# Optimization experiments

Measured on AMD Instinct MI355X. Metric: run time of the kernel, lower is better.

The kernel has to match this reference:

```python
import jax, jax.numpy as jnp
import numpy as np

N_HEAD = 12
SCALING = 0.17677669529663687  # 1/sqrt(head_dim=32)


def setup_inputs() -> dict:
    key = jax.random.key(0)
    ks = jax.random.split(key, 6)
    B, R, C, E = 1, 256, 384, 384
    s = 1.0 / np.sqrt(E)
    return {
        "x": jax.random.normal(ks[0], (B, R, C, E), dtype=jnp.float32),
        "Wq": (jax.random.normal(ks[1], (E, E), dtype=jnp.float32) * s),
        "Wk": (jax.random.normal(ks[2], (E, E), dtype=jnp.float32) * s),
        "Wv": (jax.random.normal(ks[3], (E, E), dtype=jnp.float32) * s),
        "Wq_s": (jax.random.normal(ks[4], (E, E), dtype=jnp.float32) * s),
        "Wk_s": (jax.random.normal(ks[5], (E, E), dtype=jnp.float32) * s),
        "res_mask": jnp.ones((B, C), dtype=jnp.int32),
        "seq_mask": jnp.ones((B, R), dtype=jnp.int32),
    }


def reference(x, Wq, Wk, Wv, Wq_s, Wk_s, res_mask, seq_mask):
    B, R, C, E = x.shape
    H = N_HEAD
    D = E // H
    NEG = jnp.finfo(x.dtype).min

    # ---- SeqWeightAttention: per-column attention over rows, query = row 0 ----
    scale_s = 1.0 / np.sqrt(D)
    msa = jnp.transpose(x, (0, 2, 1, 3))                 # [B,C,R,E]
    q0 = msa[:, :, 0]                                    # [B,C,E]
    Qs = (q0 @ Wq_s).reshape(B, C, 1, H, D)
    Qs = jnp.transpose(Qs, (0, 1, 3, 2, 4)) * scale_s    # [B,C,H,1,D]
    Ks = (msa @ Wk_s).reshape(B, C, R, H, D)
    Ks = jnp.transpose(Ks, (0, 1, 3, 4, 2))              # [B,C,H,D,R]
    QKs = Qs @ Ks                                        # [B,C,H,1,R]
    QKs = jnp.where(seq_mask[:, None, None, None, :] == 0, NEG, QKs)
    sw = jax.nn.softmax(QKs, axis=-1)
    sw = jnp.transpose(sw, (0, 4, 1, 2, 3))              # [B,R,C,H,1]

    # ---- main attention, row-contracted (attn_seq_weight path) ----
    scaling = SCALING / np.sqrt(C)                        # seqlen_scaling=True
    Q = (x @ Wq).reshape(B, R, C, H, D) * scaling * sw    # Q modulated by seq weights
    K = (x @ Wk).reshape(B, R, C, H, D)
    V = (x @ Wv).reshape(B, R, C, H, D)

    QK = jnp.einsum('brihd,brjhd->bhij', Q, K)            # contract rows + head_dim
    rm = res_mask[:, :, None] * res_mask[:, None, :]      # [B,C,C]
    QK = jnp.where(rm[:, None, :, :] == 0, NEG, QK)
    attn = jax.nn.softmax(QK, axis=-1)                    # [B,H,C,C]

    out = jnp.einsum('bhij,brjhd->brihd', attn, V)
    return out.reshape(B, R, C, E)
```

## Files before the change

### kernel.cpp

```cpp
#include <hip/hip_runtime.h>
#include <math.h>
#include <stdint.h>

#define DEV_INLINE __device__ __forceinline__

constexpr int R_ = 256, C_ = 384, E_ = 384, H_ = 12, D_ = 32;
constexpr float NEGF = -3.402823466e38f;

typedef __attribute__((ext_vector_type(4))) float f32x4;
typedef __attribute__((ext_vector_type(8))) short short8;
typedef __attribute__((ext_vector_type(4))) unsigned short u16x4;

constexpr size_t o_qs     = 0;
constexpr size_t o_p      = o_qs + (size_t)C_ * E_;
constexpr size_t o_logits = o_p + (size_t)C_ * H_ * E_;
constexpr size_t o_sw     = o_logits + (size_t)C_ * H_ * R_;
constexpr size_t o_attn   = o_sw + (size_t)C_ * H_ * R_;
constexpr size_t o_q3     = o_attn + (size_t)H_ * C_ * C_;
constexpr size_t SZBIG  = 75497472;
constexpr size_t ob_q3b = o_q3 * 4;
constexpr size_t ob_k3b = ob_q3b + SZBIG;
constexpr size_t ob_v3b = ob_k3b + SZBIG;
constexpr size_t ob_xb  = ob_v3b + SZBIG;

DEV_INLINE unsigned short bf16h(float x) {
  unsigned int u = __builtin_bit_cast(unsigned int, x);
  unsigned int r = (u + 0x7FFFu + ((u >> 16) & 1u)) >> 16;
  return (unsigned short)r;
}
DEV_INLINE float waveRedMax(float v) {
#pragma unroll
  for (int o = 32; o > 0; o >>= 1) v = fmaxf(v, __shfl_down(v, o));
  return v;
}
DEV_INLINE float waveRedSum(float v) {
#pragma unroll
  for (int o = 32; o > 0; o >>= 1) v += __shfl_down(v, o);
  return v;
}

DEV_INLINE void gll16(const void* g, void* l) {
  __builtin_amdgcn_global_load_lds(
      reinterpret_cast<__attribute__((address_space(1))) void*>(
          reinterpret_cast<uintptr_t>(g)),
      reinterpret_cast<__attribute__((address_space(3))) void*>(
          reinterpret_cast<uintptr_t>(l)),
      16, 0, 0);
}

template <int ROWS, int UPR, int MASK>
DEV_INLINE void stageT(const unsigned short* __restrict__ g, int lda,
                       unsigned short* l) {
  int t = threadIdx.x, w = t >> 6, lane = t & 63;
  constexpr int NI = (ROWS * UPR) / 64;
  constexpr int PW = NI / 4;
#pragma unroll
  for (int j = 0; j < PW; ++j) {
    int u0 = (w * PW + j) * 64;
    int u = u0 + lane;
    int row = u / UPR, qp = u % UPR;
    int q = qp ^ (row & MASK);
    gll16(g + (size_t)row * lda + q * 8, l + (size_t)u0 * 8);
  }
}

template <int MASK>
DEV_INLINE short8 fragLd(const unsigned short* base, int row, int q, int rowShorts) {
  int qp = q ^ (row & MASK);
  return *(const short8*)(base + row * rowShorts + qp * 8);
}

__global__ void k_qs(const float* __restrict__ x, const float* __restrict__ Wq_s,
                     float* __restrict__ ws) {
  int c = blockIdx.x, t = threadIdx.x;
  __shared__ float xl[E_];
  xl[t] = x[(size_t)c * E_ + t];
  __syncthreads();
  float s = 0.f;
#pragma unroll 8
  for (int k = 0; k < E_; ++k) s += xl[k] * Wq_s[(size_t)k * E_ + t];
  ws[o_qs + (size_t)c * E_ + t] = s * 0.17677669529663687f;
}

__global__ void k_p(const float* __restrict__ Wk_s, const float* __restrict__ ws,
                    unsigned short* __restrict__ Pb) {
  int h = blockIdx.x, c = blockIdx.y, t = threadIdx.x;
  __shared__ float q[D_];
  float s = 0.f;
  if (h < 12) {
    if (t < D_) q[t] = ws[o_qs + (size_t)c * E_ + h * D_ + t];
    __syncthreads();
    const float* wrow = &Wk_s[(size_t)t * E_ + h * D_];
#pragma unroll
    for (int d = 0; d < D_; d += 4) {
      float4 w = *(const float4*)&wrow[d];
      s += w.x * q[d] + w.y * q[d + 1] + w.z * q[d + 2] + w.w * q[d + 3];
    }
  }
  Pb[((size_t)c * 16 + h) * 384 + t] = bf16h(s);
}

__global__ __launch_bounds__(256) void k_logits_sm(
    const unsigned short* __restrict__ xb, const unsigned short* __restrict__ Pb,
    const int* __restrict__ seq_mask, float* __restrict__ swT) {
  int c = blockIdx.x, t = threadIdx.x;
  __shared__ unsigned short sA[256 * 32];
  __shared__ unsigned short sB[16 * 32];
  __shared__ float lg[12 * 256];
  __shared__ float red[4];
  int w = t >> 6, lane = t & 63, id16 = lane & 15, g = lane >> 4;
  f32x4 acc[4];
#pragma unroll
  for (int mi = 0; mi < 4; ++mi) acc[mi] = (f32x4){0.f, 0.f, 0.f, 0.f};

  for (int k0 = 0; k0 < 384; k0 += 32) {
    stageT<256, 4, 3>(xb + (size_t)c * 384 + k0, 384 * 384, sA);
    if (w == 0) {
      int row = lane >> 2, qp = lane & 3, q = qp ^ (row & 3);
      gll16(Pb + ((size_t)c * 16 + row) * 384 + k0 + q * 8, sB);
    }
    __syncthreads();
    short8 Bf = fragLd<3>(sB, id16, g, 32);
#pragma unroll
    for (int mi = 0; mi < 4; ++mi) {
      short8 Af = fragLd<3>(sA, w * 64 + mi * 16 + id16, g, 32);
      acc[mi] = __builtin_amdgcn_mfma_f32_16x16x32_bf16(Af, Bf, acc[mi], 0, 0, 0);
    }
    __syncthreads();
  }
  int l4 = (lane >> 4) * 4;
#pragma unroll
  for (int mi = 0; mi < 4; ++mi) {
    if (id16 < 12) {
      f32x4 a = acc[mi];
#pragma unroll
      for (int reg = 0; reg < 4; ++reg)
        lg[id16 * 256 + w * 64 + mi * 16 + l4 + reg] = a[reg];
    }
  }
  __syncthreads();
  int wid = t >> 6;
  const float scal = 0.17677669529663687f / sqrtf((float)C_);
  bool masked = (seq_mask[t] == 0);
  for (int h = 0; h < 12; ++h) {
    float v = masked ? NEGF : lg[h * 256 + t];
    float m = waveRedMax(v);
    if ((t & 63) == 0) red[wid] = m;
    __syncthreads();
    float mx = fmaxf(fmaxf(red[0], red[1]), fmaxf(red[2], red[3]));
    __syncthreads();
    float e = expf(v - mx);
    float s = waveRedSum(e);
    if ((t & 63) == 0) red[wid] = s;
    __syncthreads();
    float sum = red[0] + red[1] + red[2] + red[3];
    swT[((size_t)h * 256 + t) * 384 + c] = e / sum * scal;
    __syncthreads();
  }
}

__global__ void k_cvt_x(const float* __restrict__ x, unsigned short* __restrict__ xb) {
  size_t i = ((size_t)blockIdx.x * 256 + threadIdx.x) * 16;
  unsigned short h[16];
#pragma unroll
  for (int j = 0; j < 4; ++j) {
    float4 f = *(const float4*)&x[i + j * 4];
    h[j * 4 + 0] = bf16h(f.x);
    h[j * 4 + 1] = bf16h(f.y);
    h[j * 4 + 2] = bf16h(f.z);
    h[j * 4 + 3] = bf16h(f.w);
  }
  *(short8*)&xb[i] = *(const short8*)&h[0];
  *(short8*)&xb[i + 8] = *(const short8*)&h[8];
}

__global__ void k_cvt_w(const float* __restrict__ Wq, const float* __restrict__ Wk,
                        const float* __restrict__ Wv, unsigned short* __restrict__ Wtb) {
  int n = blockIdx.x, k = threadIdx.x;
  const float* W;
  int col;
  if (n < 384)      { W = Wq; col = n; }
  else if (n < 768) { W = Wk; col = n - 384; }
  else              { W = Wv; col = n - 768; }
  Wtb[(size_t)n * 384 + k] = bf16h(W[(size_t)k * 384 + col]);
}

__global__ __launch_bounds__(256, 4) void k_proj_all(
    const unsigned short* __restrict__ xb, const unsigned short* __restrict__ Wtb,
    const float* __restrict__ swT, unsigned short* __restrict__ Q3b,
    unsigned short* __restrict__ K3b, unsigned short* __restrict__ V3b) {
  __shared__ unsigned short sA[128 * 64], sB[128 * 64];
  int Dd = blockIdx.x;
  int L = (Dd & 7) * 864 + (Dd >> 3);
  int bm = L / 9, bn = L - bm * 9;
  int n0 = bn * 128, m0 = bm * 128;
  int wave = threadIdx.x >> 6, wr = wave >> 1, wc = wave & 1;
  int lane = threadIdx.x & 63, id16 = lane & 15, g = lane >> 4;
  f32x4 acc[4][4];
#pragma unroll
  for (int mi = 0; mi < 4; ++mi)
#pragma unroll
    for (int ni = 0; ni < 4; ++ni) acc[mi][ni] = (f32x4){0.f, 0.f, 0.f, 0.f};

  for (int it = 0; it < 6; ++it) {
    stageT<128, 8, 7>(xb + (size_t)m0 * 384 + it * 64, 384, sA);
    stageT<128, 8, 7>(Wtb + (size_t)n0 * 384 + it * 64, 384, sB);
    __syncthreads();
    short8 Af[4][2], Bf[4][2];
#pragma unroll
    for (int mi = 0; mi < 4; ++mi) {
      int row = wr * 64 + mi * 16 + id16;
#pragma unroll
      for (int kk = 0; kk < 2; ++kk) Af[mi][kk] = fragLd<7>(sA, row, kk * 4 + g, 64);
    }
#pragma unroll
    for (int ni = 0; ni < 4; ++ni) {
      int col = wc * 64 + ni * 16 + id16;
#pragma unroll
      for (int kk = 0; kk < 2; ++kk) Bf[ni][kk] = fragLd<7>(sB, col, kk * 4 + g, 64);
    }
#pragma unroll
    for (int kk = 0; kk < 2; ++kk)
#pragma unroll
      for (int mi = 0; mi < 4; ++mi)
#pragma unroll
        for (int ni = 0; ni < 4; ++ni)
          acc[mi][ni] = __builtin_amdgcn_mfma_f32_16x16x32_bf16(Af[mi][kk], Bf[ni][kk],
                                                                acc[mi][ni], 0, 0, 0);
    __syncthreads();
  }

  int l4 = (lane >> 4) * 4;
  int r = bm / 3, cb = (bm % 3) * 128;
  if (bn < 6) {
#pragma unroll
    for (int mi = 0; mi < 4; ++mi) {
      int cbase = cb + wr * 64 + mi * 16 + l4;
#pragma unroll
      for (int ni = 0; ni < 4; ++ni) {
        int n = n0 + wc * 64 + ni * 16 + id16;
        bool isQ = n < 384;
        int nn = isQ ? n : n - 384;
        int hh = nn >> 5, dd = nn & 31;
        f32x4 a = acc[mi][ni];
        if (isQ) {
          float4 sv = *(const float4*)&swT[((size_t)hh * 256 + r) * 384 + cbase];
          a[0] *= sv.x; a[1] *= sv.y; a[2] *= sv.z; a[3] *= sv.w;
        }
        unsigned short* dst = isQ ? Q3b : K3b;
#pragma unroll
        for (int reg = 0; reg < 4; ++reg)
          dst[((size_t)(hh * 384 + cbase + reg)) * 8192 + r * 32 + dd] = bf16h(a[reg]);
      }
    }
  } else {
#pragma unroll
    for (int mi = 0; mi < 4; ++mi) {
      int c0 = cb + wr * 64 + mi * 16 + l4;
#pragma unroll
      for (int ni = 0; ni < 4; ++ni) {
        int nv = n0 + wc * 64 + ni * 16 + id16 - 768;
        int hh = nv >> 5, dd = nv & 31;
        f32x4 a = acc[mi][ni];
        u16x4 hv;
#pragma unroll
        for (int reg = 0; reg < 4; ++reg) hv[reg] = bf16h(a[reg]);
        *(u16x4*)(V3b + ((size_t)hh * 8192 + r * 32 + dd) * 384 + c0) = hv;
      }
    }
  }
}

__global__ __launch_bounds__(256, 4) void k_qk_mma(
    const unsigned short* __restrict__ Q3b, const unsigned short* __restrict__ K3b,
    float* __restrict__ QKf0, float* __restrict__ QKf1) {
  __shared__ unsigned short sA[64 * 128], sB[64 * 128];
  int Dd = blockIdx.x;
  int L = (Dd & 7) * 108 + (Dd >> 3);
  int kh = L / 432, rem = L - kh * 432;
  int h = rem / 36, r2 = rem - h * 36, bi = r2 / 6, bj = r2 - bi * 6;
  int wave = threadIdx.x >> 6, wr = wave >> 1, wc = wave & 1;
  int lane = threadIdx.x & 63, id16 = lane & 15, g = lane >> 4;
  f32x4 acc[2][2];
#pragma unroll
  for (int mi = 0; mi < 2; ++mi)
#pragma unroll
    for (int ni = 0; ni < 2; ++ni) acc[mi][ni] = (f32x4){0.f, 0.f, 0.f, 0.f};
  const unsigned short* Ab =
      Q3b + (size_t)h * 384 * 8192 + (size_t)(bi * 64) * 8192 + kh * 4096;
  const unsigned short* Bb =
      K3b + (size_t)h * 384 * 8192 + (size_t)(bj * 64) * 8192 + kh * 4096;

  for (int it = 0; it < 32; ++it) {
    stageT<64, 16, 7>(Ab + it * 128, 8192, sA);
    stageT<64, 16, 7>(Bb + it * 128, 8192, sB);
    __syncthreads();
    short8 Af[2][4], Bf[2][4];
#pragma unroll
    for (int mi = 0; mi < 2; ++mi) {
      int row = wr * 32 + mi * 16 + id16;
#pragma unroll
      for (int kk = 0; kk < 4; ++kk) Af[mi][kk] = fragLd<7>(sA, row, kk * 4 + g, 128);
    }
#pragma unroll
    for (int ni = 0; ni < 2; ++ni) {
      int col = wc * 32 + ni * 16 + id16;
#pragma unroll
      for (int kk = 0; kk < 4; ++kk) Bf[ni][kk] = fragLd<7>(sB, col, kk * 4 + g, 128);
    }
#pragma unroll
    for (int kk = 0; kk < 4; ++kk)
#pragma unroll
      for (int mi = 0; mi < 2; ++mi)
#pragma unroll
        for (int ni = 0; ni < 2; ++ni)
          acc[mi][ni] = __builtin_amdgcn_mfma_f32_16x16x32_bf16(Af[mi][kk], Bf[ni][kk],
                                                                acc[mi][ni], 0, 0, 0);
    __syncthreads();
  }
  int l4 = (lane >> 4) * 4;
  float* dst = kh ? QKf1 : QKf0;
#pragma unroll
  for (int mi = 0; mi < 2; ++mi)
#pragma unroll
    for (int ni = 0; ni < 2; ++ni) {
      int i0 = bi * 64 + wr * 32 + mi * 16 + l4;
      int j = bj * 64 + wc * 32 + ni * 16 + id16;
      f32x4 a = acc[mi][ni];
#pragma unroll
      for (int reg = 0; reg < 4; ++reg)
        dst[((size_t)h * 384 + i0 + reg) * 384 + j] = a[reg];
    }
}

__global__ void k_softmax_j(const int* __restrict__ res_mask, const float* __restrict__ QKf0,
                            const float* __restrict__ QKf1,
                            unsigned short* __restrict__ attnb) {
  int i = blockIdx.x, h = blockIdx.y, t = threadIdx.x;
  int lane = t & 63, wid = t >> 6;
  size_t base = ((size_t)h * C_ + i) * C_;
  float v = QKf0[base + t] + QKf1[base + t];
  if ((res_mask[i] * res_mask[t]) == 0) v = NEGF;
  __shared__ float red[6];
  float m = waveRedMax(v);
  if (lane == 0) red[wid] = m;
  __syncthreads();
  float mx = red[0];
#pragma unroll
  for (int w = 1; w < 6; ++w) mx = fmaxf(mx, red[w]);
  __syncthreads();
  float e = expf(v - mx);
  float s = waveRedSum(e);
  if (lane == 0) red[wid] = s;
  __syncthreads();
  float sum = 0.f;
#pragma unroll
  for (int w = 0; w < 6; ++w) sum += red[w];
  attnb[base + t] = bf16h(e / sum);
}

__global__ __launch_bounds__(256, 4) void k_out_mma(
    const unsigned short* __restrict__ attnb, const unsigned short* __restrict__ V3b,
    float* __restrict__ out) {
  __shared__ unsigned short sA[128 * 64], sB[128 * 64];
  int Dd = blockIdx.x;
  int L = (Dd & 7) * 288 + (Dd >> 3);
  int bn = L % 64, bm = (L / 64) % 3, h = L / 192;
  int n0 = bn * 128, m0 = bm * 128;
  int wave = threadIdx.x >> 6, wr = wave >> 1, wc = wave & 1;
  int lane = threadIdx.x & 63, id16 = lane & 15, g = lane >> 4;
  f32x4 acc[4][4];
#pragma unroll
  for (int mi = 0; mi < 4; ++mi)
#pragma unroll
    for (int ni = 0; ni < 4; ++ni) acc[mi][ni] = (f32x4){0.f, 0.f, 0.f, 0.f};
  const unsigned short* Ab = attnb + (size_t)h * 384 * 384 + (size_t)m0 * 384;
  const unsigned short* Bb = V3b + (size_t)h * 8192 * 384 + (size_t)n0 * 384;

  for (int it = 0; it < 6; ++it) {
    stageT<128, 8, 7>(Ab + it * 64, 384, sA);
    stageT<128, 8, 7>(Bb + it * 64, 384, sB);
    __syncthreads();
    short8 Af[4][2], Bf[4][2];
#pragma unroll
    for (int mi = 0; mi < 4; ++mi) {
      int row = wr * 64 + mi * 16 + id16;
#pragma unroll
      for (int kk = 0; kk < 2; ++kk) Af[mi][kk] = fragLd<7>(sA, row, kk * 4 + g, 64);
    }
#pragma unroll
    for (int ni = 0; ni < 4; ++ni) {
      int col = wc * 64 + ni * 16 + id16;
#pragma unroll
      for (int kk = 0; kk < 2; ++kk) Bf[ni][kk] = fragLd<7>(sB, col, kk * 4 + g, 64);
    }
#pragma unroll
    for (int kk = 0; kk < 2; ++kk)
#pragma unroll
      for (int mi = 0; mi < 4; ++mi)
#pragma unroll
        for (int ni = 0; ni < 4; ++ni)
          acc[mi][ni] = __builtin_amdgcn_mfma_f32_16x16x32_bf16(Af[mi][kk], Bf[ni][kk],
                                                                acc[mi][ni], 0, 0, 0);
    __syncthreads();
  }
  int l4 = (lane >> 4) * 4;
#pragma unroll
  for (int mi = 0; mi < 4; ++mi)
#pragma unroll
    for (int ni = 0; ni < 4; ++ni) {
      int i0 = m0 + wr * 64 + mi * 16 + l4;
      int n = n0 + wc * 64 + ni * 16 + id16;
      int r = n >> 5, d = n & 31;
      f32x4 a = acc[mi][ni];
#pragma unroll
      for (int reg = 0; reg < 4; ++reg)
        out[(((size_t)r * 384 + i0 + reg) * 12 + h) * 32 + d] = a[reg];
    }
}

extern "C" void kernel_launch(void* const* d_in, const int* in_sizes, int n_in,
                              void* d_out, int out_size, void* d_ws, size_t ws_size,
                              hipStream_t stream) {
  const float* x = (const float*)d_in[0];
  const float* Wq = (const float*)d_in[1];
  const float* Wk = (const float*)d_in[2];
  const float* Wv = (const float*)d_in[3];
  const float* Wq_s = (const float*)d_in[4];
  const float* Wk_s = (const float*)d_in[5];
  const int* res_mask = (const int*)d_in[6];
  const int* seq_mask = (const int*)d_in[7];
  float* ws = (float*)d_ws;
  char* wsb = (char*)d_ws;
  float* out = (float*)d_out;

  unsigned short* Pb  = (unsigned short*)(wsb + o_p * 4);
  float* swT          = ws + o_logits;
  unsigned short* Wtb = (unsigned short*)(wsb + o_attn * 4);
  float* QKf0         = ws + o_attn;
  unsigned short* Q3b = (unsigned short*)(wsb + ob_q3b);
  unsigned short* K3b = (unsigned short*)(wsb + ob_k3b);
  unsigned short* V3b = (unsigned short*)(wsb + ob_v3b);
  unsigned short* xb  = (unsigned short*)(wsb + ob_xb);
  unsigned short* attnb = Q3b;
  float* QKf1 = (float*)(wsb + ob_xb);

  hipLaunchKernelGGL(k_cvt_x, dim3(9216), dim3(256), 0, stream, x, xb);
  hipLaunchKernelGGL(k_qs, dim3(C_), dim3(E_), 0, stream, x, Wq_s, ws);
  hipLaunchKernelGGL(k_p, dim3(16, C_), dim3(E_), 0, stream, Wk_s, ws, Pb);
  hipLaunchKernelGGL(k_logits_sm, dim3(C_), dim3(256), 0, stream, xb, Pb, seq_mask, swT);
  hipLaunchKernelGGL(k_cvt_w, dim3(1152), dim3(384), 0, stream, Wq, Wk, Wv, Wtb);
  hipLaunchKernelGGL(k_proj_all, dim3(6912), dim3(256), 0, stream, xb, Wtb, swT,
                     Q3b, K3b, V3b);
  hipLaunchKernelGGL(k_qk_mma, dim3(864), dim3(256), 0, stream, Q3b, K3b, QKf0, QKf1);
  hipLaunchKernelGGL(k_softmax_j, dim3(C_, H_), dim3(C_), 0, stream, res_mask,
                     QKf0, QKf1, attnb);
  hipLaunchKernelGGL(k_out_mma, dim3(2304), dim3(256), 0, stream, attnb, V3b, out);
}
```

Baseline: 411.8 us.

## Change Q/K layout to head-row-column-dim and retile QK GEMM to 128x128

The projection epilogue now stages Q and K tiles in shared memory and writes them as contiguous 16-byte chunks in an [h][r][c][d] layout instead of scattered 2-byte stores with an 8192 stride. The QK kernel is rewritten to consume that layout, using 128x128 output tiles and staging two rows of 32 head-dim values per iteration, with a shifted swizzle to suit 64-byte rows. This cuts the grid from 864 to 216 blocks, which lowers occupancy on a chip with many CUs, in exchange for more data reuse per block and coalesced projection stores.

```diff
diff --git a/kernel.cpp b/kernel.cpp
--- a/kernel.cpp
+++ b/kernel.cpp
@@ -48,7 +48,7 @@
       16, 0, 0);
 }
 
-template <int ROWS, int UPR, int MASK>
+template <int ROWS, int UPR, int MASK, int SHIFT>
 DEV_INLINE void stageT(const unsigned short* __restrict__ g, int lda,
                        unsigned short* l) {
   int t = threadIdx.x, w = t >> 6, lane = t & 63;
@@ -59,14 +59,14 @@
     int u0 = (w * PW + j) * 64;
     int u = u0 + lane;
     int row = u / UPR, qp = u % UPR;
-    int q = qp ^ (row & MASK);
+    int q = qp ^ ((row >> SHIFT) & MASK);
     gll16(g + (size_t)row * lda + q * 8, l + (size_t)u0 * 8);
   }
 }
 
-template <int MASK>
+template <int MASK, int SHIFT>
 DEV_INLINE short8 fragLd(const unsigned short* base, int row, int q, int rowShorts) {
-  int qp = q ^ (row & MASK);
+  int qp = q ^ ((row >> SHIFT) & MASK);
   return *(const short8*)(base + row * rowShorts + qp * 8);
 }
 
@@ -114,16 +114,16 @@
   for (int mi = 0; mi < 4; ++mi) acc[mi] = (f32x4){0.f, 0.f, 0.f, 0.f};
 
   for (int k0 = 0; k0 < 384; k0 += 32) {
-    stageT<256, 4, 3>(xb + (size_t)c * 384 + k0, 384 * 384, sA);
+    stageT<256, 4, 3, 0>(xb + (size_t)c * 384 + k0, 384 * 384, sA);
     if (w == 0) {
       int row = lane >> 2, qp = lane & 3, q = qp ^ (row & 3);
       gll16(Pb + ((size_t)c * 16 + row) * 384 + k0 + q * 8, sB);
     }
     __syncthreads();
-    short8 Bf = fragLd<3>(sB, id16, g, 32);
+    short8 Bf = fragLd<3, 0>(sB, id16, g, 32);
 #pragma unroll
     for (int mi = 0; mi < 4; ++mi) {
-      short8 Af = fragLd<3>(sA, w * 64 + mi * 16 + id16, g, 32);
+      short8 Af = fragLd<3, 0>(sA, w * 64 + mi * 16 + id16, g, 32);
       acc[mi] = __builtin_amdgcn_mfma_f32_16x16x32_bf16(Af, Bf, acc[mi], 0, 0, 0);
     }
     __syncthreads();
@@ -189,7 +189,9 @@
     const unsigned short* __restrict__ xb, const unsigned short* __restrict__ Wtb,
     const float* __restrict__ swT, unsigned short* __restrict__ Q3b,
     unsigned short* __restrict__ K3b, unsigned short* __restrict__ V3b) {
-  __shared__ unsigned short sA[128 * 64], sB[128 * 64];
+  __shared__ unsigned short smem[2 * 128 * 64];
+  unsigned short* sA = smem;
+  unsigned short* sB = smem + 128 * 64;
   int Dd = blockIdx.x;
   int L = (Dd & 7) * 864 + (Dd >> 3);
   int bm = L / 9, bn = L - bm * 9;
@@ -203,21 +205,21 @@
     for (int ni = 0; ni < 4; ++ni) acc[mi][ni] = (f32x4){0.f, 0.f, 0.f, 0.f};
 
   for (int it = 0; it < 6; ++it) {
-    stageT<128, 8, 7>(xb + (size_t)m0 * 384 + it * 64, 384, sA);
-    stageT<128, 8, 7>(Wtb + (size_t)n0 * 384 + it * 64, 384, sB);
+    stageT<128, 8, 7, 0>(xb + (size_t)m0 * 384 + it * 64, 384, sA);
+    stageT<128, 8, 7, 0>(Wtb + (size_t)n0 * 384 + it * 64, 384, sB);
     __syncthreads();
     short8 Af[4][2], Bf[4][2];
 #pragma unroll
     for (int mi = 0; mi < 4; ++mi) {
       int row = wr * 64 + mi * 16 + id16;
 #pragma unroll
-      for (int kk = 0; kk < 2; ++kk) Af[mi][kk] = fragLd<7>(sA, row, kk * 4 + g, 64);
+      for (int kk = 0; kk < 2; ++kk) Af[mi][kk] = fragLd<7, 0>(sA, row, kk * 4 + g, 64);
     }
 #pragma unroll
     for (int ni = 0; ni < 4; ++ni) {
       int col = wc * 64 + ni * 16 + id16;
 #pragma unroll
-      for (int kk = 0; kk < 2; ++kk) Bf[ni][kk] = fragLd<7>(sB, col, kk * 4 + g, 64);
+      for (int kk = 0; kk < 2; ++kk) Bf[ni][kk] = fragLd<7, 0>(sB, col, kk * 4 + g, 64);
     }
 #pragma unroll
     for (int kk = 0; kk < 2; ++kk)
@@ -233,30 +235,41 @@
   int l4 = (lane >> 4) * 4;
   int r = bm / 3, cb = (bm % 3) * 128;
   if (bn < 6) {
+    bool isQ = bn < 3;
+    int hbase = isQ ? bn * 4 : (bn - 3) * 4;
 #pragma unroll
     for (int mi = 0; mi < 4; ++mi) {
-      int cbase = cb + wr * 64 + mi * 16 + l4;
+      int clBase = wr * 64 + mi * 16 + l4;
 #pragma unroll
       for (int ni = 0; ni < 4; ++ni) {
-        int n = n0 + wc * 64 + ni * 16 + id16;
-        bool isQ = n < 384;
-        int nn = isQ ? n : n - 384;
-        int hh = nn >> 5, dd = nn & 31;
+        int nl = wc * 64 + ni * 16 + id16;
+        int hhl = nl >> 5, d = nl & 31;
         f32x4 a = acc[mi][ni];
         if (isQ) {
-          float4 sv = *(const float4*)&swT[((size_t)hh * 256 + r) * 384 + cbase];
+          float4 sv =
+              *(const float4*)&swT[((size_t)(hbase + hhl) * 256 + r) * 384 + cb + clBase];
           a[0] *= sv.x; a[1] *= sv.y; a[2] *= sv.z; a[3] *= sv.w;
         }
-        unsigned short* dst = isQ ? Q3b : K3b;
 #pragma unroll
         for (int reg = 0; reg < 4; ++reg)
-          dst[((size_t)(hh * 384 + cbase + reg)) * 8192 + r * 32 + dd] = bf16h(a[reg]);
+          smem[hhl * 4096 + (clBase + reg) * 32 + d] = bf16h(a[reg]);
       }
     }
+    __syncthreads();
+    unsigned short* dst = isQ ? Q3b : K3b;
+#pragma unroll
+    for (int seg = 0; seg < 8; ++seg) {
+      int off = seg * 2048 + threadIdx.x * 8;
+      int hhl = off >> 12, inner = off & 4095;
+      int hg = hbase + hhl;
+      *(short8*)(dst + (((size_t)hg * 256 + r) * 384 + cb) * 32 + inner) =
+          *(const short8*)(smem + off);
+    }
   } else {
+    int r2 = r, cb2 = cb;
 #pragma unroll
     for (int mi = 0; mi < 4; ++mi) {
-      int c0 = cb + wr * 64 + mi * 16 + l4;
+      int c0 = cb2 + wr * 64 + mi * 16 + l4;
 #pragma unroll
       for (int ni = 0; ni < 4; ++ni) {
         int nv = n0 + wc * 64 + ni * 16 + id16 - 768;
@@ -265,7 +278,7 @@
         u16x4 hv;
 #pragma unroll
         for (int reg = 0; reg < 4; ++reg) hv[reg] = bf16h(a[reg]);
-        *(u16x4*)(V3b + ((size_t)hh * 8192 + r * 32 + dd) * 384 + c0) = hv;
+        *(u16x4*)(V3b + ((size_t)hh * 8192 + r2 * 32 + dd) * 384 + c0) = hv;
       }
     }
   }
@@ -274,62 +287,60 @@
 __global__ __launch_bounds__(256, 4) void k_qk_mma(
     const unsigned short* __restrict__ Q3b, const unsigned short* __restrict__ K3b,
     float* __restrict__ QKf0, float* __restrict__ QKf1) {
-  __shared__ unsigned short sA[64 * 128], sB[64 * 128];
+  __shared__ unsigned short sA[2 * 4096], sB[2 * 4096];
   int Dd = blockIdx.x;
-  int L = (Dd & 7) * 108 + (Dd >> 3);
-  int kh = L / 432, rem = L - kh * 432;
-  int h = rem / 36, r2 = rem - h * 36, bi = r2 / 6, bj = r2 - bi * 6;
+  int L = (Dd & 7) * 27 + (Dd >> 3);
+  int kh = L / 108, rem = L - kh * 108;
+  int h = rem / 9, r2 = rem - h * 9, bi = r2 / 3, bj = r2 - bi * 3;
+  int i0 = bi * 128, j0 = bj * 128;
   int wave = threadIdx.x >> 6, wr = wave >> 1, wc = wave & 1;
   int lane = threadIdx.x & 63, id16 = lane & 15, g = lane >> 4;
-  f32x4 acc[2][2];
-#pragma unroll
-  for (int mi = 0; mi < 2; ++mi)
-#pragma unroll
-    for (int ni = 0; ni < 2; ++ni) acc[mi][ni] = (f32x4){0.f, 0.f, 0.f, 0.f};
-  const unsigned short* Ab =
-      Q3b + (size_t)h * 384 * 8192 + (size_t)(bi * 64) * 8192 + kh * 4096;
-  const unsigned short* Bb =
-      K3b + (size_t)h * 384 * 8192 + (size_t)(bj * 64) * 8192 + kh * 4096;
-
-  for (int it = 0; it < 32; ++it) {
-    stageT<64, 16, 7>(Ab + it * 128, 8192, sA);
-    stageT<64, 16, 7>(Bb + it * 128, 8192, sB);
-    __syncthreads();
-    short8 Af[2][4], Bf[2][4];
-#pragma unroll
-    for (int mi = 0; mi < 2; ++mi) {
-      int row = wr * 32 + mi * 16 + id16;
-#pragma unroll
-      for (int kk = 0; kk < 4; ++kk) Af[mi][kk] = fragLd<7>(sA, row, kk * 4 + g, 128);
-    }
-#pragma unroll
-    for (int ni = 0; ni < 2; ++ni) {
-      int col = wc * 32 + ni * 16 + id16;
-#pragma unroll
-      for (int kk = 0; kk < 4; ++kk) Bf[ni][kk] = fragLd<7>(sB, col, kk * 4 + g, 128);
-    }
-#pragma unroll
-    for (int kk = 0; kk < 4; ++kk)
-#pragma unroll
-      for (int mi = 0; mi < 2; ++mi)
-#pragma unroll
-        for (int ni = 0; ni < 2; ++ni)
-          acc[mi][ni] = __builtin_amdgcn_mfma_f32_16x16x32_bf16(Af[mi][kk], Bf[ni][kk],
+  f32x4 acc[4][4];
+#pragma unroll
+  for (int mi = 0; mi < 4; ++mi)
+#pragma unroll
+    for (int ni = 0; ni < 4; ++ni) acc[mi][ni] = (f32x4){0.f, 0.f, 0.f, 0.f};
+
+  for (int it = 0; it < 64; ++it) {
+    int r = kh * 128 + it * 2;
+#pragma unroll
+    for (int rr = 0; rr < 2; ++rr) {
+      stageT<128, 4, 3, 1>(Q3b + (((size_t)h * 256 + r + rr) * 384 + i0) * 32, 32,
+                           sA + rr * 4096);
+      stageT<128, 4, 3, 1>(K3b + (((size_t)h * 256 + r + rr) * 384 + j0) * 32, 32,
+                           sB + rr * 4096);
+    }
+    __syncthreads();
+#pragma unroll
+    for (int rr = 0; rr < 2; ++rr) {
+      short8 Af[4], Bf[4];
+#pragma unroll
+      for (int mi = 0; mi < 4; ++mi)
+        Af[mi] = fragLd<3, 1>(sA + rr * 4096, wr * 64 + mi * 16 + id16, g, 32);
+#pragma unroll
+      for (int ni = 0; ni < 4; ++ni)
+        Bf[ni] = fragLd<3, 1>(sB + rr * 4096, wc * 64 + ni * 16 + id16, g, 32);
+#pragma unroll
+      for (int mi = 0; mi < 4; ++mi)
+#pragma unroll
+        for (int ni = 0; ni < 4; ++ni)
+          acc[mi][ni] = __builtin_amdgcn_mfma_f32_16x16x32_bf16(Af[mi], Bf[ni],
                                                                 acc[mi][ni], 0, 0, 0);
+    }
     __syncthreads();
   }
   int l4 = (lane >> 4) * 4;
   float* dst = kh ? QKf1 : QKf0;
 #pragma unroll
-  for (int mi = 0; mi < 2; ++mi)
-#pragma unroll
-    for (int ni = 0; ni < 2; ++ni) {
-      int i0 = bi * 64 + wr * 32 + mi * 16 + l4;
-      int j = bj * 64 + wc * 32 + ni * 16 + id16;
+  for (int mi = 0; mi < 4; ++mi)
+#pragma unroll
+    for (int ni = 0; ni < 4; ++ni) {
+      int ii = i0 + wr * 64 + mi * 16 + l4;
+      int j = j0 + wc * 64 + ni * 16 + id16;
       f32x4 a = acc[mi][ni];
 #pragma unroll
       for (int reg = 0; reg < 4; ++reg)
-        dst[((size_t)h * 384 + i0 + reg) * 384 + j] = a[reg];
+        dst[((size_t)h * 384 + ii + reg) * 384 + j] = a[reg];
     }
 }
 
@@ -378,21 +389,21 @@
   const unsigned short* Bb = V3b + (size_t)h * 8192 * 384 + (size_t)n0 * 384;
 
   for (int it = 0; it < 6; ++it) {
-    stageT<128, 8, 7>(Ab + it * 64, 384, sA);
-    stageT<128, 8, 7>(Bb + it * 64, 384, sB);
+    stageT<128, 8, 7, 0>(Ab + it * 64, 384, sA);
+    stageT<128, 8, 7, 0>(Bb + it * 64, 384, sB);
     __syncthreads();
     short8 Af[4][2], Bf[4][2];
 #pragma unroll
     for (int mi = 0; mi < 4; ++mi) {
       int row = wr * 64 + mi * 16 + id16;
 #pragma unroll
-      for (int kk = 0; kk < 2; ++kk) Af[mi][kk] = fragLd<7>(sA, row, kk * 4 + g, 64);
+      for (int kk = 0; kk < 2; ++kk) Af[mi][kk] = fragLd<7, 0>(sA, row, kk * 4 + g, 64);
     }
 #pragma unroll
     for (int ni = 0; ni < 4; ++ni) {
       int col = wc * 64 + ni * 16 + id16;
 #pragma unroll
-      for (int kk = 0; kk < 2; ++kk) Bf[ni][kk] = fragLd<7>(sB, col, kk * 4 + g, 64);
+      for (int kk = 0; kk < 2; ++kk) Bf[ni][kk] = fragLd<7, 0>(sB, col, kk * 4 + g, 64);
     }
 #pragma unroll
     for (int kk = 0; kk < 2; ++kk)
@@ -452,7 +463,7 @@
   hipLaunchKernelGGL(k_cvt_w, dim3(1152), dim3(384), 0, stream, Wq, Wk, Wv, Wtb);
   hipLaunchKernelGGL(k_proj_all, dim3(6912), dim3(256), 0, stream, xb, Wtb, swT,
                      Q3b, K3b, V3b);
-  hipLaunchKernelGGL(k_qk_mma, dim3(864), dim3(256), 0, stream, Q3b, K3b, QKf0, QKf1);
+  hipLaunchKernelGGL(k_qk_mma, dim3(216), dim3(256), 0, stream, Q3b, K3b, QKf0, QKf1);
   hipLaunchKernelGGL(k_softmax_j, dim3(C_, H_), dim3(C_), 0, stream, res_mask,
                      QKf0, QKf1, attnb);
   hipLaunchKernelGGL(k_out_mma, dim3(2304), dim3(256), 0, stream, attnb, V3b, out);
```

Measured after the change: 399.5 us. -3.0%, faster.
